# Kernel optimization log

Hardware: AMD Instinct MI355X
Metric: run time of the kernel (lower is better)

The kernel has to match this reference:

```python
import jax, jax.numpy as jnp
import numpy as np

E = 1024   # embedding_dim
H = 16     # num_head
D = 64     # dim_head (E == H*D)
R = 8      # LoRA rank
BATCH = 2
SEQ = 2048
EPS = 1e-6


def setup_inputs() -> dict:
    key = jax.random.key(0)
    ks = jax.random.split(key, 16)
    s = 0.02
    return {
        "y": jax.random.normal(ks[0], (BATCH, SEQ, E), jnp.float32),
        "Wqkv": jax.random.normal(ks[1], (3 * E, E), jnp.float32) * s,
        "bqkv": jax.random.normal(ks[2], (3 * E,), jnp.float32) * s,
        "Wmsa": jax.random.normal(ks[3], (E, E), jnp.float32) * s,
        "Bq": jax.random.normal(ks[4], (E, R), jnp.float32) * s,
        "Aq": jax.random.normal(ks[5], (R, E), jnp.float32) * s,
        "Bk": jax.random.normal(ks[6], (E, R), jnp.float32) * s,
        "Ak": jax.random.normal(ks[7], (R, E), jnp.float32) * s,
        "Bv": jax.random.normal(ks[8], (E, R), jnp.float32) * s,
        "Av": jax.random.normal(ks[9], (R, E), jnp.float32) * s,
        "Bo": jax.random.normal(ks[10], (E, R), jnp.float32) * s,
        "Ao": jax.random.normal(ks[11], (R, E), jnp.float32) * s,
        "gamma": jnp.ones((E,), jnp.float32),
        "beta": jnp.zeros((E,), jnp.float32),
        "i": 0,
    }


def reference(y, Wqkv, bqkv, Wmsa, Bq, Aq, Bk, Ak, Bv, Av, Bo, Ao, gamma, beta, i):
    B, S, En = y.shape
    # fused QKV projection: nn.Linear -> y @ W.T + b
    qkv = (y @ Wqkv.T + bqkv).reshape(B, S, 3, H, D).transpose(2, 0, 3, 1, 4)
    Q, K, V = qkv[0], qkv[1], qkv[2]          # each [B,H,S,D]

    def lora_delta(Bw, Aw):
        # torch: y @ (B.weight @ A.weight), reshaped to heads
        return (y @ (Bw @ Aw)).reshape(B, S, H, D).transpose(0, 2, 1, 3)

    Q = Q + lora_delta(Bq, Aq)
    K = K + lora_delta(Bk, Ak)
    V = V + lora_delta(Bv, Av)

    scale = jnp.asarray(np.sqrt(D), y.dtype)
    scores = jnp.einsum('bhqd,bhkd->bhqk', Q, K) / scale
    attn = jax.nn.softmax(scores, axis=-1)
    o = jnp.einsum('bhqk,bhkd->bhqd', attn, V)          # [B,H,S,D]
    o = o.transpose(0, 2, 1, 3).reshape(B, S, H * D)    # [B,S,E]

    msa = o @ Wmsa.T + o @ (Bo @ Ao)
    res = msa + y

    mu = jnp.mean(res, axis=-1, keepdims=True)
    var = jnp.var(res, axis=-1, keepdims=True)
    return (res - mu) * jax.lax.rsqrt(var + EPS) * gamma + beta
```

## Files before the change

### kernel.cpp

```cpp
#include <hip/hip_runtime.h>
#include <hip/hip_bf16.h>
#include <stdint.h>

typedef __attribute__((ext_vector_type(8))) short short8;
typedef __attribute__((ext_vector_type(4))) float f32x4;

typedef const __attribute__((address_space(1))) void gv_t;
typedef __attribute__((address_space(3))) void lv_t;

#define SCQ 0.18033688011112042f

__device__ __forceinline__ void gl_lds16(const void* g, void* l) {
    __builtin_amdgcn_global_load_lds((gv_t*)g, (lv_t*)l, 16, 0, 0);
}

__device__ __forceinline__ unsigned short f2bf(float f) {
    union { float f; unsigned int u; } v; v.f = f;
    unsigned int r = v.u + 0x7fffu + ((v.u >> 16) & 1u);
    return (unsigned short)(r >> 16);
}

__device__ __forceinline__ unsigned int pack2bf(float a, float b) {
    union { __hip_bfloat162 h2; unsigned int u; } cv;
    cv.h2 = __float22bfloat162_rn(make_float2(a, b));
    return cv.u;
}

__device__ __forceinline__ f32x4 zero4() { f32x4 z = {0.f, 0.f, 0.f, 0.f}; return z; }

__global__ void k_prep(const float* __restrict__ y,
                       const float* __restrict__ Wqkv, const float* __restrict__ Wmsa,
                       const float* __restrict__ Bq, const float* __restrict__ Aq,
                       const float* __restrict__ Bk, const float* __restrict__ Ak,
                       const float* __restrict__ Bv, const float* __restrict__ Av,
                       const float* __restrict__ Bo, const float* __restrict__ Ao,
                       unsigned short* __restrict__ wout, unsigned short* __restrict__ yb) {
    const int bid = blockIdx.x;
    if (bid < 16384) {
        int idx = bid * 256 + threadIdx.x;
        int n = idx >> 10, k = idx & 1023;
        int sel = n >> 10, n0 = n & 1023;
        const float* Bp = (sel == 0) ? Bq : (sel == 1) ? Bk : (sel == 2) ? Bv : Bo;
        const float* Ap = (sel == 0) ? Aq : (sel == 1) ? Ak : (sel == 2) ? Av : Ao;
        float acc = (sel < 3) ? Wqkv[idx] : Wmsa[idx - 3145728];
        float4 b0 = *(const float4*)(Bp + k * 8);
        float4 b1 = *(const float4*)(Bp + k * 8 + 4);
        acc += b0.x * Ap[0 * 1024 + n0] + b0.y * Ap[1 * 1024 + n0]
             + b0.z * Ap[2 * 1024 + n0] + b0.w * Ap[3 * 1024 + n0]
             + b1.x * Ap[4 * 1024 + n0] + b1.y * Ap[5 * 1024 + n0]
             + b1.z * Ap[6 * 1024 + n0] + b1.w * Ap[7 * 1024 + n0];
        wout[idx] = f2bf(acc * ((sel == 0) ? SCQ : 1.0f));
    } else {
        int i = ((bid - 16384) * 256 + threadIdx.x) * 4;
        float4 v = *(const float4*)(y + i);
        union { unsigned short u[4]; uint2 w; } o;
        o.u[0] = f2bf(v.x); o.u[1] = f2bf(v.y); o.u[2] = f2bf(v.z); o.u[3] = f2bf(v.w);
        *(uint2*)(yb + i) = o.w;
    }
}

template <int TM, int EPI, int MINW, int XMAP>
__global__ __launch_bounds__(256, MINW) void k_gemm(const unsigned short* __restrict__ Ag,
                                                    const unsigned short* __restrict__ Bg,
                                                    const float* __restrict__ bias,
                                                    const float* __restrict__ yres,
                                                    unsigned short* __restrict__ vtg,
                                                    void* __restrict__ Cout,
                                                    int M, int N, int K) {
    constexpr int WAVES_N = 256 / TM;
    constexpr int WN = TM / 2;
    constexpr int NI = WN / 16;
    constexpr int ACALLS = TM / 64;
    constexpr int ASZ = 2 * TM * 32;
    __shared__ unsigned short SH[ASZ + 2 * 128 * 32];
    unsigned short* As0 = SH;
    unsigned short* Bs0 = SH + ASZ;
    const int flat = threadIdx.x;
    int m0, n0;
    if constexpr (XMAP == 1) {
        int id = blockIdx.x, xcd = id & 7, j = id >> 3;
        int yy = (xcd & 3) * 8 + j / 12;
        int xx = (xcd >> 2) * 12 + j % 12;
        m0 = yy * TM; n0 = xx * 128;
    } else if constexpr (XMAP == 2) {
        int id = blockIdx.x, xcd = id & 7, j = id >> 3;
        int yy = xcd * 8 + j / 8;
        int xx = j % 8;
        m0 = yy * TM; n0 = xx * 128;
    } else {
        m0 = blockIdx.y * TM; n0 = blockIdx.x * 128;
    }
    const int lane = flat & 63, wave = flat >> 6;
    const int l16 = lane & 15, quad = lane >> 4;
    const int wm = (wave / WAVES_N) * 64, wn = (wave % WAVES_N) * WN;

    f32x4 acc[4][NI];
    #pragma unroll
    for (int mi = 0; mi < 4; ++mi)
        #pragma unroll
        for (int ni = 0; ni < NI; ++ni) acc[mi][ni] = zero4();

    const unsigned short* ap = Ag + (size_t)(m0 + (flat >> 2)) * K + (flat & 3) * 8;
    const unsigned short* bp = Bg + (size_t)(n0 + (flat >> 2)) * K + (flat & 3) * 8;
    const size_t rstep = (size_t)64 * K;

    #pragma unroll
    for (int c = 0; c < ACALLS; ++c) gl_lds16(ap + c * rstep, &As0[c * 2048 + flat * 8]);
    gl_lds16(bp,         &Bs0[flat * 8]);
    gl_lds16(bp + rstep, &Bs0[2048 + flat * 8]);
    ap += 32; bp += 32;
    __syncthreads();

    for (int k0 = 0; k0 < K; k0 += 32) {
        const int cur = (k0 >> 5) & 1;
        if (k0 + 32 < K) {
            const int nxt = cur ^ 1;
            #pragma unroll
            for (int c = 0; c < ACALLS; ++c) gl_lds16(ap + c * rstep, &As0[nxt * TM * 32 + c * 2048 + flat * 8]);
            gl_lds16(bp,         &Bs0[nxt * 4096 + flat * 8]);
            gl_lds16(bp + rstep, &Bs0[nxt * 4096 + 2048 + flat * 8]);
            ap += 32; bp += 32;
        }

        short8 af[4], bfr[NI];
        #pragma unroll
        for (int i = 0; i < 4; ++i) af[i] = *(const short8*)&As0[cur * TM * 32 + (wm + i * 16 + l16) * 32 + quad * 8];
        #pragma unroll
        for (int i = 0; i < NI; ++i) bfr[i] = *(const short8*)&Bs0[cur * 4096 + (wn + i * 16 + l16) * 32 + quad * 8];
        #pragma unroll
        for (int mi = 0; mi < 4; ++mi)
            #pragma unroll
            for (int ni = 0; ni < NI; ++ni)
                acc[mi][ni] = __builtin_amdgcn_mfma_f32_16x16x32_bf16(af[mi], bfr[ni], acc[mi][ni], 0, 0, 0);

        __syncthreads();
    }

    if (EPI == 0) {
        unsigned short* C = (unsigned short*)Cout;
        if (n0 < 2048) {
            #pragma unroll
            for (int ni = 0; ni < NI; ++ni) {
                int col = n0 + wn + ni * 16 + l16;
                float bv = bias[col] * ((col < 1024) ? SCQ : 1.0f);
                #pragma unroll
                for (int mi = 0; mi < 4; ++mi) {
                    int row = m0 + wm + mi * 16 + quad * 4;
                    #pragma unroll
                    for (int r = 0; r < 4; ++r)
                        C[(size_t)(row + r) * N + col] = f2bf(acc[mi][ni][r] + bv);
                }
            }
        } else {
            if constexpr (TM == 128) {
                #pragma unroll
                for (int ni = 0; ni < NI; ++ni) {
                    int c = wn + ni * 16 + l16;
                    float bv = bias[n0 + c];
                    int sw = (c & 7) << 3;
                    #pragma unroll
                    for (int mi = 0; mi < 4; ++mi) {
                        int row = wm + mi * 16 + quad * 4;
                        uint2 w;
                        w.x = pack2bf(acc[mi][ni][0] + bv, acc[mi][ni][1] + bv);
                        w.y = pack2bf(acc[mi][ni][2] + bv, acc[mi][ni][3] + bv);
                        *(uint2*)&SH[c * 128 + (row ^ sw)] = w;
                    }
                }
                __syncthreads();
                const int bb = m0 >> 11, ss = m0 & 2047;
                #pragma unroll
                for (int p = 0; p < 4; ++p) {
                    int c = p * 32 + (flat >> 3);
                    int col = n0 + c;
                    int hh = (col - 2048) >> 6, dd = col & 63;
                    unsigned short* dst = vtg + (size_t)(hh * 64 + dd) * 2048
                                              + (size_t)bb * 2097152 + ss;
                    int sw = (c & 7) << 3;
                    #pragma unroll
                    for (int hf = 0; hf < 2; ++hf) {
                        int off = hf * 64 + (flat & 7) * 8;
                        uint4 v = *(const uint4*)&SH[c * 128 + (off ^ sw)];
                        *(uint4*)(dst + off) = v;
                    }
                }
            }
        }
    } else {
        float* C = (float*)Cout;
        #pragma unroll
        for (int ni = 0; ni < NI; ++ni) {
            int col = n0 + wn + ni * 16 + l16;
            #pragma unroll
            for (int mi = 0; mi < 4; ++mi) {
                int row = m0 + wm + mi * 16 + quad * 4;
                #pragma unroll
                for (int r = 0; r < 4; ++r)
                    C[(size_t)(row + r) * N + col] = acc[mi][ni][r] + yres[(size_t)(row + r) * N + col];
            }
        }
    }
}

__global__ __launch_bounds__(256, 2) void k_attn(const unsigned short* __restrict__ qkv,
                                                 const unsigned short* __restrict__ vtg,
                                                 unsigned short* __restrict__ o) {
    __shared__ unsigned short LDS[16384];
    unsigned short* Qs = LDS;
    unsigned short* Ks0 = LDS;
    unsigned short* Vt0 = LDS + 8192;

    const int t = threadIdx.x;
    const int lane = t & 63, wave = t >> 6;
    const int l16 = lane & 15, quad = lane >> 4;
    const int l8 = l16 & 7;
    const int id = blockIdx.x;
    const int xcd = id & 7, loc = id >> 3;
    const int qb = loc & 15;
    const int P = xcd + 8 * (loc >> 4);
    const int h = P & 15, b = P >> 4;
    const int q0 = qb * 128;

    const unsigned short* qbase = qkv + (size_t)(b * 2048) * 3072 + h * 64;
    const unsigned short* kbase = qbase + 1024;
    const unsigned short* vtbase = vtg + (size_t)((b * 16 + h) * 64) * 2048;

    #pragma unroll
    for (int i = 0; i < 4; ++i) {
        int B = i * 256 + t;
        int row = B >> 3, c = (B & 7) ^ (row & 7);
        gl_lds16(qbase + (size_t)(q0 + row) * 3072 + c * 8, &Qs[B * 8]);
    }

    const int B0 = t, B1 = t + 256;
    const int r0 = B0 >> 3, c0 = (B0 & 7) ^ (r0 & 7);
    const int r1 = B1 >> 3, c1 = (B1 & 7) ^ (r1 & 7);
    const unsigned short* kp0 = kbase + (size_t)r0 * 3072 + c0 * 8;
    const unsigned short* kp1 = kbase + (size_t)r1 * 3072 + c1 * 8;
    const unsigned short* vp0 = vtbase + (size_t)r0 * 2048 + c0 * 8;
    const unsigned short* vp1 = vtbase + (size_t)r1 * 2048 + c1 * 8;

    __syncthreads();

    short8 qf[2][2];
    #pragma unroll
    for (int ni = 0; ni < 2; ++ni)
        #pragma unroll
        for (int kk = 0; kk < 2; ++kk)
            qf[ni][kk] = *(const short8*)&Qs[(wave * 32 + ni * 16 + l16) * 64 + ((kk * 4 + quad) ^ l8) * 8];

    __syncthreads();

    gl_lds16(kp0, &Ks0[B0 * 8]);
    gl_lds16(kp1, &Ks0[B1 * 8]);
    gl_lds16(vp0, &Vt0[B0 * 8]);
    gl_lds16(vp1, &Vt0[B1 * 8]);
    kp0 += 64 * 3072; kp1 += 64 * 3072; vp0 += 64; vp1 += 64;

    f32x4 acc_o[2][4];
    #pragma unroll
    for (int mo = 0; mo < 2; ++mo)
        #pragma unroll
        for (int nd = 0; nd < 4; ++nd) acc_o[mo][nd] = zero4();
    f32x4 acc_l[2] = {zero4(), zero4()};
    const f32x4 Z4 = zero4();
    short8 ones;
    #pragma unroll
    for (int i = 0; i < 8; ++i) ones[i] = (short)0x3F80;

    __syncthreads();

    for (int j = 0; j < 32; ++j) {
        const unsigned short* Ks = Ks0 + (j & 1) * 4096;
        const unsigned short* Vt = Vt0 + (j & 1) * 4096;

        if (j < 31) {
            unsigned short* Kn = Ks0 + ((j + 1) & 1) * 4096;
            unsigned short* Vn = Vt0 + ((j + 1) & 1) * 4096;
            gl_lds16(kp0, &Kn[B0 * 8]);
            gl_lds16(kp1, &Kn[B1 * 8]);
            gl_lds16(vp0, &Vn[B0 * 8]);
            gl_lds16(vp1, &Vn[B1 * 8]);
            kp0 += 64 * 3072; kp1 += 64 * 3072; vp0 += 64; vp1 += 64;
        }

        f32x4 sacc[4][2];
        #pragma unroll
        for (int mi = 0; mi < 4; ++mi) {
            short8 kf0 = *(const short8*)&Ks[(mi * 16 + l16) * 64 + ((0 + quad) ^ l8) * 8];
            short8 kf1 = *(const short8*)&Ks[(mi * 16 + l16) * 64 + ((4 + quad) ^ l8) * 8];
            #pragma unroll
            for (int ni = 0; ni < 2; ++ni) {
                sacc[mi][ni] = __builtin_amdgcn_mfma_f32_16x16x32_bf16(kf0, qf[ni][0], Z4, 0, 0, 0);
                sacc[mi][ni] = __builtin_amdgcn_mfma_f32_16x16x32_bf16(kf1, qf[ni][1], sacc[mi][ni], 0, 0, 0);
            }
        }

        short8 pf[2][2];
        #pragma unroll
        for (int ni = 0; ni < 2; ++ni)
            #pragma unroll
            for (int kk = 0; kk < 2; ++kk) {
                float e00 = __builtin_amdgcn_exp2f(sacc[2 * kk][ni][0]);
                float e01 = __builtin_amdgcn_exp2f(sacc[2 * kk][ni][1]);
                float e02 = __builtin_amdgcn_exp2f(sacc[2 * kk][ni][2]);
                float e03 = __builtin_amdgcn_exp2f(sacc[2 * kk][ni][3]);
                float e10 = __builtin_amdgcn_exp2f(sacc[2 * kk + 1][ni][0]);
                float e11 = __builtin_amdgcn_exp2f(sacc[2 * kk + 1][ni][1]);
                float e12 = __builtin_amdgcn_exp2f(sacc[2 * kk + 1][ni][2]);
                float e13 = __builtin_amdgcn_exp2f(sacc[2 * kk + 1][ni][3]);
                unsigned int a0 = pack2bf(e00, e01);
                unsigned int b0 = pack2bf(e10, e11);
                unsigned int a1 = pack2bf(e02, e03);
                unsigned int b1 = pack2bf(e12, e13);
                asm volatile("v_permlane32_swap_b32 %0, %1\n\t"
                             "v_permlane16_swap_b32 %0, %1"
                             : "+v"(a0), "+v"(b0));
                asm volatile("v_permlane32_swap_b32 %0, %1\n\t"
                             "v_permlane16_swap_b32 %0, %1"
                             : "+v"(a1), "+v"(b1));
                union { unsigned int u[4]; short8 s; } cv;
                cv.u[0] = a0; cv.u[1] = a1; cv.u[2] = b0; cv.u[3] = b1;
                pf[ni][kk] = cv.s;
            }

        #pragma unroll
        for (int kk = 0; kk < 2; ++kk) {
            #pragma unroll
            for (int mo = 0; mo < 2; ++mo)
                acc_l[mo] = __builtin_amdgcn_mfma_f32_16x16x32_bf16(pf[mo][kk], ones, acc_l[mo], 0, 0, 0);
            #pragma unroll
            for (int nd = 0; nd < 4; ++nd) {
                short8 vf = *(const short8*)&Vt[(nd * 16 + l16) * 64 + ((kk * 4 + quad) ^ l8) * 8];
                #pragma unroll
                for (int mo = 0; mo < 2; ++mo)
                    acc_o[mo][nd] = __builtin_amdgcn_mfma_f32_16x16x32_bf16(pf[mo][kk], vf, acc_o[mo][nd], 0, 0, 0);
            }
        }

        __syncthreads();
    }

    #pragma unroll
    for (int mo = 0; mo < 2; ++mo)
        #pragma unroll
        for (int rr = 0; rr < 4; ++rr) {
            float inv = 1.0f / acc_l[mo][rr];
            int qg = q0 + wave * 32 + mo * 16 + quad * 4 + rr;
            size_t base = ((size_t)(b * 2048 + qg)) * 1024 + h * 64;
            #pragma unroll
            for (int nd = 0; nd < 4; ++nd)
                o[base + nd * 16 + l16] = f2bf(acc_o[mo][nd][rr] * inv);
        }
}

__global__ __launch_bounds__(256) void k_ln(const float* __restrict__ res,
                                            const float* __restrict__ g,
                                            const float* __restrict__ be,
                                            float* __restrict__ out) {
    const int row = blockIdx.x * 4 + (threadIdx.x >> 6);
    const int lane = threadIdx.x & 63;
    const float* x = res + (size_t)row * 1024;
    float4 v[4];
    float s = 0.f, sq = 0.f;
    #pragma unroll
    for (int i = 0; i < 4; ++i) {
        v[i] = *(const float4*)(x + i * 256 + lane * 4);
        s  += v[i].x + v[i].y + v[i].z + v[i].w;
        sq += v[i].x * v[i].x + v[i].y * v[i].y + v[i].z * v[i].z + v[i].w * v[i].w;
    }
    #pragma unroll
    for (int off = 32; off; off >>= 1) { s += __shfl_down(s, off); sq += __shfl_down(sq, off); }
    s = __shfl(s, 0); sq = __shfl(sq, 0);
    float mu = s * (1.f / 1024.f);
    float var = sq * (1.f / 1024.f) - mu * mu;
    float rstd = rsqrtf(var + 1e-6f);
    float* orow = out + (size_t)row * 1024;
    #pragma unroll
    for (int i = 0; i < 4; ++i) {
        float4 gg = *(const float4*)(g + i * 256 + lane * 4);
        float4 bb = *(const float4*)(be + i * 256 + lane * 4);
        float4 ov;
        ov.x = (v[i].x - mu) * rstd * gg.x + bb.x;
        ov.y = (v[i].y - mu) * rstd * gg.y + bb.y;
        ov.z = (v[i].z - mu) * rstd * gg.z + bb.z;
        ov.w = (v[i].w - mu) * rstd * gg.w + bb.w;
        *(float4*)(orow + i * 256 + lane * 4) = ov;
    }
}

extern "C" void kernel_launch(void* const* d_in, const int* in_sizes, int n_in,
                              void* d_out, int out_size, void* d_ws, size_t ws_size,
                              hipStream_t stream) {
    (void)in_sizes; (void)n_in; (void)out_size; (void)ws_size;
    const float* y    = (const float*)d_in[0];
    const float* Wqkv = (const float*)d_in[1];
    const float* bqkv = (const float*)d_in[2];
    const float* Wmsa = (const float*)d_in[3];
    const float* Bq = (const float*)d_in[4];
    const float* Aq = (const float*)d_in[5];
    const float* Bk = (const float*)d_in[6];
    const float* Ak = (const float*)d_in[7];
    const float* Bv = (const float*)d_in[8];
    const float* Av = (const float*)d_in[9];
    const float* Bo = (const float*)d_in[10];
    const float* Ao = (const float*)d_in[11];
    const float* gamma = (const float*)d_in[12];
    const float* beta  = (const float*)d_in[13];

    char* ws = (char*)d_ws;
    unsigned short* yb   = (unsigned short*)(ws);
    unsigned short* weq  = (unsigned short*)(ws + (8u  << 20));
    unsigned short* qkv  = (unsigned short*)(ws + (16u << 20));
    unsigned short* vtg  = (unsigned short*)(ws + (40u << 20));
    unsigned short* wem  = weq + 3145728;
    unsigned short* obuf = yb;
    float* res = (float*)qkv;

    k_prep<<<17408, 256, 0, stream>>>(y, Wqkv, Wmsa, Bq, Aq, Bk, Ak, Bv, Av, Bo, Ao, weq, yb);
    k_gemm<128, 0, 3, 1><<<768, 256, 0, stream>>>(yb, weq, bqkv, nullptr, vtg, (void*)qkv, 4096, 3072, 1024);
    k_attn<<<512, 256, 0, stream>>>(qkv, vtg, obuf);
    k_gemm<64, 1, 4, 2><<<512, 256, 0, stream>>>(obuf, wem, nullptr, y, nullptr, (void*)res, 4096, 1024, 1024);
    k_ln  <<<1024, 256, 0, stream>>>(res, gamma, beta, (float*)d_out);
}
```

Baseline: 209.7 us.

## Split-K the output projection GEMM and fold residual add into LayerNorm

The output projection GEMM changes from 64-row tiles with full K to 128-row tiles split into two K halves of 512. The halves are spread across XCD groups, and each writes a separate bf16 partial buffer. LayerNorm now reads y plus both bf16 partials and sums them before normalising, so the fp32 residual round-trip goes away. This keeps 512 blocks with larger tiles and shorter K loops, but rounding the partials to bf16 costs some accuracy and adds a second partial read in LayerNorm.

Result: no change. 208.0 us (-0.8%).

```diff
diff --git a/kernel.cpp b/kernel.cpp
--- a/kernel.cpp
+++ b/kernel.cpp
@@ -18,6 +18,10 @@
     union { float f; unsigned int u; } v; v.f = f;
     unsigned int r = v.u + 0x7fffu + ((v.u >> 16) & 1u);
     return (unsigned short)(r >> 16);
+}
+
+__device__ __forceinline__ float bf2f(unsigned short u) {
+    union { unsigned int i; float f; } v; v.i = ((unsigned int)u) << 16; return v.f;
 }
 
 __device__ __forceinline__ unsigned int pack2bf(float a, float b) {
@@ -66,7 +70,7 @@
                                                     const float* __restrict__ yres,
                                                     unsigned short* __restrict__ vtg,
                                                     void* __restrict__ Cout,
-                                                    int M, int N, int K) {
+                                                    int M, int N, int K, int Kst) {
     constexpr int WAVES_N = 256 / TM;
     constexpr int WN = TM / 2;
     constexpr int NI = WN / 16;
@@ -76,7 +80,7 @@
     unsigned short* As0 = SH;
     unsigned short* Bs0 = SH + ASZ;
     const int flat = threadIdx.x;
-    int m0, n0;
+    int m0, n0, koff = 0, split = 0;
     if constexpr (XMAP == 1) {
         int id = blockIdx.x, xcd = id & 7, j = id >> 3;
         int yy = (xcd & 3) * 8 + j / 12;
@@ -84,9 +88,10 @@
         m0 = yy * TM; n0 = xx * 128;
     } else if constexpr (XMAP == 2) {
         int id = blockIdx.x, xcd = id & 7, j = id >> 3;
-        int yy = xcd * 8 + j / 8;
-        int xx = j % 8;
-        m0 = yy * TM; n0 = xx * 128;
+        split = xcd >> 2;
+        int yy = (xcd & 3) * 8 + (j >> 3);
+        int xx = j & 7;
+        m0 = yy * TM; n0 = xx * 128; koff = split * 512;
     } else {
         m0 = blockIdx.y * TM; n0 = blockIdx.x * 128;
     }
@@ -100,9 +105,9 @@
         #pragma unroll
         for (int ni = 0; ni < NI; ++ni) acc[mi][ni] = zero4();
 
-    const unsigned short* ap = Ag + (size_t)(m0 + (flat >> 2)) * K + (flat & 3) * 8;
-    const unsigned short* bp = Bg + (size_t)(n0 + (flat >> 2)) * K + (flat & 3) * 8;
-    const size_t rstep = (size_t)64 * K;
+    const unsigned short* ap = Ag + (size_t)(m0 + (flat >> 2)) * Kst + koff + (flat & 3) * 8;
+    const unsigned short* bp = Bg + (size_t)(n0 + (flat >> 2)) * Kst + koff + (flat & 3) * 8;
+    const size_t rstep = (size_t)64 * Kst;
 
     #pragma unroll
     for (int c = 0; c < ACALLS; ++c) gl_lds16(ap + c * rstep, &As0[c * 2048 + flat * 8]);
@@ -136,7 +141,7 @@
         __syncthreads();
     }
 
-    if (EPI == 0) {
+    if constexpr (EPI == 0) {
         unsigned short* C = (unsigned short*)Cout;
         if (n0 < 2048) {
             #pragma unroll
@@ -186,7 +191,7 @@
                 }
             }
         }
-    } else {
+    } else if constexpr (EPI == 1) {
         float* C = (float*)Cout;
         #pragma unroll
         for (int ni = 0; ni < NI; ++ni) {
@@ -197,6 +202,19 @@
                 #pragma unroll
                 for (int r = 0; r < 4; ++r)
                     C[(size_t)(row + r) * N + col] = acc[mi][ni][r] + yres[(size_t)(row + r) * N + col];
+            }
+        }
+    } else {
+        unsigned short* C = (unsigned short*)Cout + (size_t)split * 4194304;
+        #pragma unroll
+        for (int ni = 0; ni < NI; ++ni) {
+            int col = n0 + wn + ni * 16 + l16;
+            #pragma unroll
+            for (int mi = 0; mi < 4; ++mi) {
+                int row = m0 + wm + mi * 16 + quad * 4;
+                #pragma unroll
+                for (int r = 0; r < 4; ++r)
+                    C[(size_t)(row + r) * N + col] = f2bf(acc[mi][ni][r]);
             }
         }
     }
@@ -354,18 +372,29 @@
         }
 }
 
-__global__ __launch_bounds__(256) void k_ln(const float* __restrict__ res,
+__global__ __launch_bounds__(256) void k_ln(const float* __restrict__ y,
+                                            const unsigned short* __restrict__ p0,
+                                            const unsigned short* __restrict__ p1,
                                             const float* __restrict__ g,
                                             const float* __restrict__ be,
                                             float* __restrict__ out) {
     const int row = blockIdx.x * 4 + (threadIdx.x >> 6);
     const int lane = threadIdx.x & 63;
-    const float* x = res + (size_t)row * 1024;
+    const float* xr = y + (size_t)row * 1024;
+    const unsigned short* ar = p0 + (size_t)row * 1024;
+    const unsigned short* br = p1 + (size_t)row * 1024;
     float4 v[4];
     float s = 0.f, sq = 0.f;
     #pragma unroll
     for (int i = 0; i < 4; ++i) {
-        v[i] = *(const float4*)(x + i * 256 + lane * 4);
+        float4 vy = *(const float4*)(xr + i * 256 + lane * 4);
+        union { uint2 w; unsigned short u[4]; } ua, ub;
+        ua.w = *(const uint2*)(ar + i * 256 + lane * 4);
+        ub.w = *(const uint2*)(br + i * 256 + lane * 4);
+        v[i].x = vy.x + bf2f(ua.u[0]) + bf2f(ub.u[0]);
+        v[i].y = vy.y + bf2f(ua.u[1]) + bf2f(ub.u[1]);
+        v[i].z = vy.z + bf2f(ua.u[2]) + bf2f(ub.u[2]);
+        v[i].w = vy.w + bf2f(ua.u[3]) + bf2f(ub.u[3]);
         s  += v[i].x + v[i].y + v[i].z + v[i].w;
         sq += v[i].x * v[i].x + v[i].y * v[i].y + v[i].z * v[i].z + v[i].w * v[i].w;
     }
@@ -415,11 +444,11 @@
     unsigned short* vtg  = (unsigned short*)(ws + (40u << 20));
     unsigned short* wem  = weq + 3145728;
     unsigned short* obuf = yb;
-    float* res = (float*)qkv;
+    unsigned short* resb = qkv;
 
     k_prep<<<17408, 256, 0, stream>>>(y, Wqkv, Wmsa, Bq, Aq, Bk, Ak, Bv, Av, Bo, Ao, weq, yb);
-    k_gemm<128, 0, 3, 1><<<768, 256, 0, stream>>>(yb, weq, bqkv, nullptr, vtg, (void*)qkv, 4096, 3072, 1024);
+    k_gemm<128, 0, 3, 1><<<768, 256, 0, stream>>>(yb, weq, bqkv, nullptr, vtg, (void*)qkv, 4096, 3072, 1024, 1024);
     k_attn<<<512, 256, 0, stream>>>(qkv, vtg, obuf);
-    k_gemm<64, 1, 4, 2><<<512, 256, 0, stream>>>(obuf, wem, nullptr, y, nullptr, (void*)res, 4096, 1024, 1024);
-    k_ln  <<<1024, 256, 0, stream>>>(res, gamma, beta, (float*)d_out);
-}
+    k_gemm<128, 2, 3, 2><<<512, 256, 0, stream>>>(obuf, wem, nullptr, nullptr, nullptr, (void*)resb, 4096, 1024, 512, 1024);
+    k_ln  <<<1024, 256, 0, stream>>>(y, resb, resb + 4194304, gamma, beta, (float*)d_out);
+}
```
